# Performance work log

Hardware: AMD Instinct MI355X
Metric: run time of the kernel (lower is better)

## Reference

```python
import jax, jax.numpy as jnp
import numpy as np

RESO = 64            # plane_resolution
PADDING = 0.1
HID = 128            # hidden_dim
CDIM = 128           # c_dim
NBLOCKS = 5
PLANES = ((0, 2), (0, 1), (1, 2))  # xz, xy, yz column picks


def _plane_index(p, cols):
    # normalize_coordinate + coordinate2index (2d)
    xy = p[..., list(cols)] / (1.0 + PADDING + 1e-3) + 0.5
    xy = jnp.clip(xy, 0.0, 1.0 - 1e-3)
    ij = (xy * RESO).astype(jnp.int32)
    return ij[..., 0] + RESO * ij[..., 1]  # [B, T]


def _flat_idx(idx, S):
    B = idx.shape[0]
    return (idx + jnp.arange(B, dtype=idx.dtype)[:, None] * S).reshape(-1)


def _scatter_max(src, idx, S):
    # src [B,T,F], idx [B,T] -> [B,S,F]; empty bins -> 0 (torch_scatter convention)
    B, T, F = src.shape
    m = jax.ops.segment_max(src.reshape(B * T, F), _flat_idx(idx, S), num_segments=B * S)
    m = jnp.where(jnp.isfinite(m), m, jnp.zeros((), src.dtype))
    return m.reshape(B, S, F)


def _scatter_mean(src, idx, S):
    B, T, F = src.shape
    flat = _flat_idx(idx, S)
    s = jax.ops.segment_sum(src.reshape(B * T, F), flat, num_segments=B * S)
    cnt = jax.ops.segment_sum(jnp.ones((B * T,), src.dtype), flat, num_segments=B * S)
    return (s / jnp.maximum(cnt, 1.0)[:, None]).reshape(B, S, F)


def _resblock(x, w0, b0, w1, b1, ws):
    # ONet ResnetBlockFC: fc_1(relu(fc_0(relu(x)))) + shortcut(x)
    net = jax.nn.relu(x) @ w0 + b0
    dx = jax.nn.relu(net) @ w1 + b1
    return x @ ws + dx


def setup_inputs() -> dict:
    key = jax.random.key(0)
    ks = jax.random.split(key, 10)
    sc = 0.05
    return {
        "p": jax.random.normal(ks[0], (8, 20000, 3), dtype=jnp.float32),
        "fc_pos_w": jax.random.normal(ks[1], (3, 2 * HID), dtype=jnp.float32) * sc,
        "fc_pos_b": jnp.zeros((2 * HID,), jnp.float32),
        "blk0_w": jax.random.normal(ks[2], (NBLOCKS, 2 * HID, HID), dtype=jnp.float32) * sc,
        "blk0_b": jnp.zeros((NBLOCKS, HID), jnp.float32),
        "blk1_w": jax.random.normal(ks[3], (NBLOCKS, HID, HID), dtype=jnp.float32) * sc,
        "blk1_b": jnp.zeros((NBLOCKS, HID), jnp.float32),
        "blk_sc_w": jax.random.normal(ks[4], (NBLOCKS, 2 * HID, HID), dtype=jnp.float32) * sc,
        "fc_c_w": jax.random.normal(ks[5], (HID, CDIM), dtype=jnp.float32) * sc,
        "fc_c_b": jnp.zeros((CDIM,), jnp.float32),
    }


def reference(p, fc_pos_w, fc_pos_b, blk0_w, blk0_b, blk1_w, blk1_b, blk_sc_w, fc_c_w, fc_c_b):
    S = RESO * RESO
    B = p.shape[0]
    idxs = [_plane_index(p, cols) for cols in PLANES]

    net = p @ fc_pos_w + fc_pos_b                         # [B,T,2H]
    net = _resblock(net, blk0_w[0], blk0_b[0], blk1_w[0], blk1_b[0], blk_sc_w[0])
    for i in range(1, NBLOCKS):
        pooled = jnp.zeros_like(net[..., :HID])
        for idx in idxs:
            fea = _scatter_max(net, idx, S)               # [B,S,H]
            pooled = pooled + jnp.take_along_axis(fea, idx[:, :, None], axis=1)
        net = jnp.concatenate([net, pooled], axis=-1)     # [B,T,2H]
        net = _resblock(net, blk0_w[i], blk0_b[i], blk1_w[i], blk1_b[i], blk_sc_w[i])

    c = net @ fc_c_w + fc_c_b                             # [B,T,C]
    feas = []
    for idx in idxs:
        fp = _scatter_mean(c, idx, S)                     # [B,S,C]
        feas.append(fp.transpose(0, 2, 1).reshape(B, CDIM, RESO, RESO))
    return jnp.stack(feas)                                # [3,B,C,R,R] (xz, xy, yz)
```

## Files before the change

### kernel.cpp

```cpp
#include <hip/hip_runtime.h>
#include <cstdint>
#include <cstddef>

#define NP     160000
#define NB     8
#define TPB    20000
#define H      128
#define SS     4096
#define NCHUNK 625
#define NBLK   10
#define PPB    2000
#define NTILE  2500
#define GRIDP  1024

typedef _Float16 half8  __attribute__((ext_vector_type(8)));
typedef _Float16 half4v __attribute__((ext_vector_type(4)));
typedef float    f32x16 __attribute__((ext_vector_type(16)));

__device__ __forceinline__ half8 reluh8(half8 x) {
  half8 z = (half8)(_Float16)0;
  return __builtin_elementwise_max(x, z);
}

__global__ __launch_bounds__(256) void k_hist(const float* __restrict__ p,
                                              int* __restrict__ idx,
                                              unsigned* __restrict__ hist) {
  __shared__ unsigned lh[SS];
  const int tid = threadIdx.x;
  const int plb = blockIdx.x % 24;
  const int blk = blockIdx.x / 24;
  const int pl = plb >> 3, b = plb & 7;
  for (int j = tid; j < SS; j += 256) lh[j] = 0;
  __syncthreads();
  const float DEN = (float)(1.0 + 0.1 + 1e-3);
  const float HI  = (float)(1.0 - 1e-3);
  const int nbase = b*TPB + blk*PPB;
  for (int j = tid; j < PPB; j += 256) {
    const int n = nbase + j;
    const float px = p[3*n], py = p[3*n+1], pz = p[3*n+2];
    float ca, cb;
    if (pl == 0)      { ca = px; cb = pz; }
    else if (pl == 1) { ca = px; cb = py; }
    else              { ca = py; cb = pz; }
    const float na = fminf(fmaxf(ca / DEN + 0.5f, 0.0f), HI);
    const float nb = fminf(fmaxf(cb / DEN + 0.5f, 0.0f), HI);
    const int bin = (int)(na * 64.0f) + 64 * (int)(nb * 64.0f);
    idx[pl*NP + n] = bin;
    atomicAdd(&lh[bin], 1u);
  }
  __syncthreads();
  unsigned* dst = hist + ((size_t)plb*NBLK + blk)*SS;
  for (int j = tid; j < SS; j += 256) dst[j] = lh[j];
}

__global__ __launch_bounds__(256) void k_scan2(unsigned* __restrict__ hist,
                                               unsigned* __restrict__ cnt,
                                               int* __restrict__ cursor) {
  __shared__ unsigned stot[SS];
  __shared__ unsigned ssum[256];
  __shared__ unsigned sbase[256];
  const int plb = blockIdx.x;
  const int tid = threadIdx.x;
  unsigned* hp = hist + (size_t)plb*NBLK*SS;
  for (int j = tid; j < SS; j += 256) {
    unsigned t = 0;
    #pragma unroll
    for (int blk = 0; blk < NBLK; ++blk) t += hp[blk*SS + j];
    stot[j] = t;
  }
  __syncthreads();
  unsigned local = 0;
  #pragma unroll
  for (int i = 0; i < 16; ++i) local += stot[tid*16 + i];
  ssum[tid] = local;
  __syncthreads();
  if (tid == 0) {
    unsigned run = 0;
    for (int i = 0; i < 256; ++i) { sbase[i] = run; run += ssum[i]; }
  }
  __syncthreads();
  unsigned run = sbase[tid];
  for (int i = 0; i < 16; ++i) {
    const int bin = tid*16 + i;
    const unsigned tot = stot[bin];
    cnt[plb*SS + bin] = tot;
    cursor[plb*SS + bin] = (int)(run + tot);
    unsigned acc = run;
    #pragma unroll
    for (int blk = 0; blk < NBLK; ++blk) {
      const unsigned c = hp[blk*SS + bin];
      hp[blk*SS + bin] = acc;
      acc += c;
    }
    run += tot;
  }
}

__global__ __launch_bounds__(256) void k_reorder2(const int* __restrict__ idx,
                                                  const unsigned* __restrict__ hist,
                                                  int* __restrict__ order) {
  __shared__ unsigned lrank[SS];
  const int tid = threadIdx.x;
  const int plb = blockIdx.x % 24;
  const int blk = blockIdx.x / 24;
  const int pl = plb >> 3, b = plb & 7;
  for (int j = tid; j < SS; j += 256) lrank[j] = 0;
  __syncthreads();
  const unsigned* bp = hist + ((size_t)plb*NBLK + blk)*SS;
  int* op = order + pl*NP + b*TPB;
  const int nbase = b*TPB + blk*PPB;
  for (int j = tid; j < PPB; j += 256) {
    const int n = nbase + j;
    const int bin = idx[pl*NP + n];
    const unsigned r = atomicAdd(&lrank[bin], 1u);
    op[bp[bin] + r] = (bin << 18) | n;
  }
}

__global__ __launch_bounds__(256) void k_wconv(const float* __restrict__ w0,
                                               const float* __restrict__ w1,
                                               const float* __restrict__ wsc,
                                               _Float16* __restrict__ wb) {
  int t = blockIdx.x*256 + threadIdx.x;
  if (t >= 51200) return;
  int L = t / 10240, r = t % 10240;
  const float* src; _Float16* dst; int q;
  if (r < 4096)      { q = r;        src = w0  + L*32768; dst = wb + L*81920;         }
  else if (r < 8192) { q = r - 4096; src = wsc + L*32768; dst = wb + L*81920 + 32768; }
  else               { q = r - 8192; src = w1  + L*16384; dst = wb + L*81920 + 65536; }
  int kt = q >> 8, nt = (q >> 6) & 3, l = q & 63;
  int k0 = kt*16 + ((l >> 5) << 3);
  int n  = nt*32 + (l & 31);
  union { _Float16 h[8]; uint4 u; } o;
  #pragma unroll
  for (int j = 0; j < 8; ++j) o.h[j] = (_Float16)src[(size_t)(k0 + j)*H + n];
  *(uint4*)(dst + (size_t)q*8) = o.u;
}

template<int OP>
__global__ __launch_bounds__(256) void k_poolA(const _Float16* __restrict__ net,
                                               const int* __restrict__ order,
                                               _Float16* __restrict__ fea,
                                               float* __restrict__ sums,
                                               float* __restrict__ pbufF,
                                               float* __restrict__ pbufL) {
  const int tid   = threadIdx.x;
  const int plb   = blockIdx.x % 24;
  const int chunk = (blockIdx.x / 24) * 8 + (tid >> 5);
  if (chunk >= NCHUNK) return;
  const int gi = tid & 31, f4 = gi << 2;
  const int pl = plb >> 3, b = plb & 7;
  const int base = pl*NP + b*TPB + chunk*32;
  const int pkv = order[base + gi];
  const int prevbin = (chunk > 0)          ? (order[base - 1] >> 18) : -1;
  const int nextbin = (chunk < NCHUNK - 1) ? (order[base + 32] >> 18) : -1;

  uint2 v[32];
  #pragma unroll
  for (int i = 0; i < 32; ++i) {
    const int pk = __shfl(pkv, i, 32);
    v[i] = *(const uint2*)&net[(size_t)(pk & 0x3FFFF)*H + f4];
  }
  __builtin_amdgcn_sched_barrier(0);

  const size_t pslot = ((size_t)plb*NCHUNK + chunk)*H + f4;
  int cur = __shfl(pkv, 0, 32) >> 18;
  int segstart = 0;
  float a0, a1, a2, a3;
  if (OP == 0) { a0 = a1 = a2 = a3 = -3.0e38f; } else { a0 = a1 = a2 = a3 = 0.f; }

  #pragma unroll
  for (int i = 0; i < 32; ++i) {
    const int bin = __shfl(pkv, i, 32) >> 18;
    if (bin != cur) {
      const bool contin = (segstart == 0) && (prevbin == cur);
      if (!contin) {
        if (OP == 0) {
          union { _Float16 h[4]; uint2 u; } o;
          o.h[0]=(_Float16)a0; o.h[1]=(_Float16)a1; o.h[2]=(_Float16)a2; o.h[3]=(_Float16)a3;
          *(uint2*)&fea[((size_t)plb*SS + cur)*H + f4] = o.u;
        } else {
          *(float4*)&sums[((size_t)plb*SS + cur)*H + f4] = make_float4(a0,a1,a2,a3);
        }
      } else {
        *(float4*)&pbufF[pslot] = make_float4(a0,a1,a2,a3);
      }
      cur = bin; segstart = i;
      if (OP == 0) { a0 = a1 = a2 = a3 = -3.0e38f; } else { a0 = a1 = a2 = a3 = 0.f; }
    }
    union { uint2 u; _Float16 h[4]; } w;
    w.u = v[i];
    if (OP == 0) {
      a0 = fmaxf(a0, (float)w.h[0]); a1 = fmaxf(a1, (float)w.h[1]);
      a2 = fmaxf(a2, (float)w.h[2]); a3 = fmaxf(a3, (float)w.h[3]);
    } else {
      a0 += (float)w.h[0]; a1 += (float)w.h[1];
      a2 += (float)w.h[2]; a3 += (float)w.h[3];
    }
  }
  const bool contin = (segstart == 0) && (prevbin == cur);
  const bool extend = (nextbin == cur);
  if (!contin && !extend) {
    if (OP == 0) {
      union { _Float16 h[4]; uint2 u; } o;
      o.h[0]=(_Float16)a0; o.h[1]=(_Float16)a1; o.h[2]=(_Float16)a2; o.h[3]=(_Float16)a3;
      *(uint2*)&fea[((size_t)plb*SS + cur)*H + f4] = o.u;
    } else {
      *(float4*)&sums[((size_t)plb*SS + cur)*H + f4] = make_float4(a0,a1,a2,a3);
    }
  } else if (contin) {
    *(float4*)&pbufF[pslot] = make_float4(a0,a1,a2,a3);
  } else {
    *(float4*)&pbufL[pslot] = make_float4(a0,a1,a2,a3);
  }
}

template<int OP>
__global__ __launch_bounds__(256) void k_poolB(const int* __restrict__ order,
                                               const int* __restrict__ cursor,
                                               _Float16* __restrict__ fea,
                                               float* __restrict__ sums,
                                               const float* __restrict__ pbufF,
                                               const float* __restrict__ pbufL) {
  const int tid = threadIdx.x;
  const int plb = blockIdx.x % 24;
  const int bnd = (blockIdx.x / 24) * 8 + (tid >> 5);
  if (bnd >= NCHUNK - 1) return;
  const int gi = tid & 31, f4 = gi << 2;
  const int pl = plb >> 3, b = plb & 7;
  const int base = pl*NP + b*TPB;
  const int pos  = (bnd + 1) * 32;
  const int binR = order[base + pos] >> 18;
  const int binL = order[base + pos - 1] >> 18;
  if (binL != binR) return;
  const int beta = binR;
  const int e = cursor[plb*SS + beta];
  const int s = (beta > 0) ? cursor[plb*SS + beta - 1] : 0;
  const int cs = s >> 5, ce = (e - 1) >> 5;
  if (cs != bnd) return;
  float4 acc = *(const float4*)&pbufL[((size_t)plb*NCHUNK + cs)*H + f4];
  #pragma unroll 4
  for (int c = cs + 1; c <= ce; ++c) {
    const float4 q = *(const float4*)&pbufF[((size_t)plb*NCHUNK + c)*H + f4];
    if (OP == 0) {
      acc.x = fmaxf(acc.x, q.x); acc.y = fmaxf(acc.y, q.y);
      acc.z = fmaxf(acc.z, q.z); acc.w = fmaxf(acc.w, q.w);
    } else {
      acc.x += q.x; acc.y += q.y; acc.z += q.z; acc.w += q.w;
    }
  }
  if (OP == 0) {
    union { _Float16 h[4]; uint2 u; } o;
    o.h[0]=(_Float16)acc.x; o.h[1]=(_Float16)acc.y;
    o.h[2]=(_Float16)acc.z; o.h[3]=(_Float16)acc.w;
    *(uint2*)&fea[((size_t)plb*SS + beta)*H + f4] = o.u;
  } else {
    *(float4*)&sums[((size_t)plb*SS + beta)*H + f4] = acc;
  }
}

template<int MODE>
__global__ __launch_bounds__(256, 4) void k_block(
    const float* __restrict__ p,
    const float* __restrict__ wpos, const float* __restrict__ bpos,
    _Float16* __restrict__ net,
    const _Float16* __restrict__ fea, const int* __restrict__ idx,
    const _Float16* __restrict__ wb,
    const float* __restrict__ b0, const float* __restrict__ b1)
{
  __shared__ char smem[32768];
  char* Xs = smem;
  char* Hs = smem;
  const int tid = threadIdx.x;

  const int w  = tid >> 6;
  const int ln = tid & 63;
  const int l5 = ln >> 5;
  const int lr = ln & 31;
  const int sw = lr << 4;
  const int a0b = lr*512 + l5*16;
  const int a1b = a0b + 32*512;
  const int col = w*32 + lr;
  const int sw1 = (lr & 15) << 4;
  const float bb0 = b0[col];
  const float bb1 = b1[col];
  const _Float16* wb0 = wb;
  const _Float16* wbs = wb + 32768;
  const _Float16* wb1 = wb + 65536;

  for (int t = blockIdx.x; t < NTILE; t += gridDim.x) {
    const int n0 = t * 64;
    if (t != (int)blockIdx.x) __syncthreads();

    if (MODE == 0) {
      for (int j = tid; j < 64*64; j += 256) {
        int pt = j >> 6, k4 = (j & 63) << 2;
        int n = n0 + pt;
        float px = p[3*n], py = p[3*n+1], pz = p[3*n+2];
        float4 a  = *(const float4*)&bpos[k4];
        float4 wx = *(const float4*)&wpos[k4];
        float4 wy = *(const float4*)&wpos[256 + k4];
        float4 wz = *(const float4*)&wpos[512 + k4];
        a.x += px*wx.x + py*wy.x + pz*wz.x;
        a.y += px*wx.y + py*wy.y + pz*wz.y;
        a.z += px*wx.z + py*wy.z + pz*wz.z;
        a.w += px*wx.w + py*wy.w + pz*wz.w;
        union { _Float16 h[4]; uint2 u; } o;
        o.h[0] = (_Float16)a.x; o.h[1] = (_Float16)a.y;
        o.h[2] = (_Float16)a.z; o.h[3] = (_Float16)a.w;
        *(uint2*)(Xs + ((pt*512 + k4*2) ^ ((pt & 31) << 4))) = o.u;
      }
    } else {
      for (int j = tid; j < 64*32; j += 256) {
        int pt = j >> 5, k4 = (j & 31) << 2;
        int n = n0 + pt;
        int b = n / TPB;
        uint2 vleft = *(const uint2*)&net[(size_t)n*H + k4];
        union { uint2 u; half4v h; } w0g, w1g, w2g, o;
        w0g.u = *(const uint2*)&fea[(((size_t)(0*NB + b))*SS + idx[0*NP + n])*H + k4];
        w1g.u = *(const uint2*)&fea[(((size_t)(1*NB + b))*SS + idx[1*NP + n])*H + k4];
        w2g.u = *(const uint2*)&fea[(((size_t)(2*NB + b))*SS + idx[2*NP + n])*H + k4];
        o.h = (w0g.h + w1g.h) + w2g.h;
        const int swp = (pt & 31) << 4;
        *(uint2*)(Xs + ((pt*512 + k4*2) ^ swp)) = vleft;
        *(uint2*)(Xs + ((pt*512 + 256 + k4*2) ^ swp)) = o.u;
      }
    }
    __syncthreads();

    f32x16 aR0 = {}, aR1 = {}, aS0 = {}, aS1 = {};

    #pragma unroll 4
    for (int kt = 0; kt < 16; ++kt) {
      half8 x0 = *(const half8*)(Xs + ((a0b + kt*32) ^ sw));
      half8 x1 = *(const half8*)(Xs + ((a1b + kt*32) ^ sw));
      half8 r0 = reluh8(x0);
      half8 r1 = reluh8(x1);
      half8 bw = *(const half8*)(wb0 + ((kt*4 + w)*64 + ln)*8);
      half8 bs = *(const half8*)(wbs + ((kt*4 + w)*64 + ln)*8);
      aR0 = __builtin_amdgcn_mfma_f32_32x32x16_f16(r0, bw, aR0, 0, 0, 0);
      aR1 = __builtin_amdgcn_mfma_f32_32x32x16_f16(r1, bw, aR1, 0, 0, 0);
      aS0 = __builtin_amdgcn_mfma_f32_32x32x16_f16(x0, bs, aS0, 0, 0, 0);
      aS1 = __builtin_amdgcn_mfma_f32_32x32x16_f16(x1, bs, aS1, 0, 0, 0);
    }
    __syncthreads();

    #pragma unroll
    for (int reg = 0; reg < 16; ++reg) {
      int ro = (reg & 3) + 8*(reg >> 2) + 4*l5;
      float v0 = fmaxf(aR0[reg] + bb0, 0.f);
      float v1 = fmaxf(aR1[reg] + bb0, 0.f);
      *(_Float16*)(Hs + ((ro*256 + col*2) ^ ((ro & 15) << 4)))      = (_Float16)v0;
      *(_Float16*)(Hs + (((32+ro)*256 + col*2) ^ ((ro & 15) << 4))) = (_Float16)v1;
    }
    __syncthreads();

    #pragma unroll 2
    for (int kt = 0; kt < 8; ++kt) {
      half8 h0 = *(const half8*)(Hs + ((lr*256 + l5*16 + kt*32) ^ sw1));
      half8 h1 = *(const half8*)(Hs + (((32+lr)*256 + l5*16 + kt*32) ^ sw1));
      half8 bf = *(const half8*)(wb1 + ((kt*4 + w)*64 + ln)*8);
      aS0 = __builtin_amdgcn_mfma_f32_32x32x16_f16(h0, bf, aS0, 0, 0, 0);
      aS1 = __builtin_amdgcn_mfma_f32_32x32x16_f16(h1, bf, aS1, 0, 0, 0);
    }

    #pragma unroll
    for (int reg = 0; reg < 16; ++reg) {
      int ro = (reg & 3) + 8*(reg >> 2) + 4*l5;
      net[(size_t)(n0 + ro)*H + col]      = (_Float16)(aS0[reg] + bb1);
      net[(size_t)(n0 + 32 + ro)*H + col] = (_Float16)(aS1[reg] + bb1);
    }
  }
}

__global__ __launch_bounds__(256) void k_out2(const float* __restrict__ sums,
                                              const unsigned* __restrict__ cnt,
                                              const float* __restrict__ wc,
                                              const float* __restrict__ bc,
                                              float* __restrict__ out) {
  __shared__ float xa[64][132];
  const int plb = blockIdx.y;
  const int s0  = blockIdx.x << 6;
  const int tid = threadIdx.x;

  for (int j = tid; j < 64*32; j += 256) {
    int si = j >> 5, k4 = (j & 31) << 2;
    int s = s0 + si;
    float4 v = *(const float4*)&sums[((size_t)plb*SS + s)*H + k4];
    unsigned c = cnt[(size_t)plb*SS + s];
    float m = (c > 0u) ? (1.0f / (float)c) : 0.0f;
    xa[si][k4+0] = v.x*m; xa[si][k4+1] = v.y*m;
    xa[si][k4+2] = v.z*m; xa[si][k4+3] = v.w*m;
  }
  __syncthreads();

  const int fg = tid & 31;
  const int pg = tid >> 5;
  const int f4c = fg << 2;
  const int prow = pg << 3;
  float ac[8][4];
  #pragma unroll
  for (int i = 0; i < 8; ++i) { ac[i][0]=ac[i][1]=ac[i][2]=ac[i][3]=0.f; }
  #pragma unroll 4
  for (int k = 0; k < H; ++k) {
    const float4 wv = *(const float4*)&wc[(size_t)k*H + f4c];
    #pragma unroll
    for (int i = 0; i < 8; ++i) {
      const float xv = xa[prow + i][k];
      ac[i][0] += xv*wv.x; ac[i][1] += xv*wv.y; ac[i][2] += xv*wv.z; ac[i][3] += xv*wv.w;
    }
  }
  __syncthreads();
  const float4 bv = *(const float4*)&bc[f4c];
  #pragma unroll
  for (int i = 0; i < 8; ++i) {
    float4 o;
    o.x = ac[i][0] + bv.x;
    o.y = ac[i][1] + bv.y;
    o.z = ac[i][2] + bv.z;
    o.w = ac[i][3] + bv.w;
    *(float4*)&xa[prow + i][f4c] = o;
  }
  __syncthreads();

  for (int j = tid; j < H * 16; j += 256) {
    const int ch = j >> 4;
    const int s4 = (j & 15) << 2;
    float4 o;
    o.x = xa[s4 + 0][ch];
    o.y = xa[s4 + 1][ch];
    o.z = xa[s4 + 2][ch];
    o.w = xa[s4 + 3][ch];
    *(float4*)&out[((size_t)plb*H + ch)*SS + s0 + s4] = o;
  }
}

extern "C" void kernel_launch(void* const* d_in, const int* in_sizes, int n_in,
                              void* d_out, int out_size, void* d_ws, size_t ws_size,
                              hipStream_t stream) {
  (void)in_sizes; (void)n_in; (void)out_size; (void)ws_size;
  const float* p      = (const float*)d_in[0];
  const float* wpos   = (const float*)d_in[1];
  const float* bpos   = (const float*)d_in[2];
  const float* blk0w  = (const float*)d_in[3];
  const float* blk0b  = (const float*)d_in[4];
  const float* blk1w  = (const float*)d_in[5];
  const float* blk1b  = (const float*)d_in[6];
  const float* blkscw = (const float*)d_in[7];
  const float* wc     = (const float*)d_in[8];
  const float* bc     = (const float*)d_in[9];
  float* out = (float*)d_out;

  char* ws = (char*)d_ws;
  _Float16* net  = (_Float16*)ws;
  int* idx       = (int*)(ws + 40960000);
  int* order     = (int*)(ws + 42880000);
  int* cursor    = (int*)(ws + 44800000);
  unsigned* cnt  = (unsigned*)(ws + 45193216);
  _Float16* wb   = (_Float16*)(ws + 45586432);
  float* sums    = (float*)(ws + 46405632);
  float* pbufF   = (float*)(ws + 96737280);
  float* pbufL   = (float*)(ws + 104417280);
  unsigned* hist = (unsigned*)(ws + 112097280);
  _Float16* fea  = (_Float16*)d_out;

  k_hist<<<24*NBLK, 256, 0, stream>>>(p, idx, hist);
  k_scan2<<<24, 256, 0, stream>>>(hist, cnt, cursor);
  k_reorder2<<<24*NBLK, 256, 0, stream>>>(idx, hist, order);
  k_wconv<<<200, 256, 0, stream>>>(blk0w, blk1w, blkscw, wb);

  k_block<0><<<GRIDP, 256, 0, stream>>>(p, wpos, bpos, net, nullptr, idx,
                                        wb, blk0b, blk1b);

  for (int i = 1; i < 5; ++i) {
    k_poolA<0><<<79*24, 256, 0, stream>>>(net, order, fea, nullptr, pbufF, pbufL);
    k_poolB<0><<<78*24, 256, 0, stream>>>(order, cursor, fea, nullptr, pbufF, pbufL);
    k_block<1><<<GRIDP, 256, 0, stream>>>(nullptr, nullptr, nullptr, net, fea, idx,
                                          wb + (size_t)i*81920,
                                          blk0b + (size_t)i*H,
                                          blk1b + (size_t)i*H);
  }

  k_poolA<1><<<79*24, 256, 0, stream>>>(net, order, nullptr, sums, pbufF, pbufL);
  k_poolB<1><<<78*24, 256, 0, stream>>>(order, cursor, nullptr, sums, pbufF, pbufL);
  k_out2<<<dim3(64, 24), 256, 0, stream>>>(sums, cnt, wc, bc, out);
}
```

Measured before the change: 519.5 us.

## Restructure resblock kernel to one tile per 512-thread block with 8 waves

Replaces the persistent grid-stride k_block (256 threads, 4 waves each computing 64 rows with two accumulator pairs) with one 64-point tile per 512-thread block, where 8 waves each own a 32x32 output sub-tile. Separate LDS regions for X and H remove one barrier, and the fc_0 result is written to H before the shortcut GEMM runs. The aim is to cut per-wave register pressure and raise occupancy and latency hiding. In exchange every wave reloads the X tile for both GEMMs, LDS use grows to 48KB per block, and there are more block launches with no weight reuse across tiles.

```diff
diff --git a/kernel.cpp b/kernel.cpp
--- a/kernel.cpp
+++ b/kernel.cpp
@@ -10,8 +10,6 @@
 #define NCHUNK 625
 #define NBLK   10
 #define PPB    2000
-#define NTILE  2500
-#define GRIDP  1024
 
 typedef _Float16 half8  __attribute__((ext_vector_type(8)));
 typedef _Float16 half4v __attribute__((ext_vector_type(4)));
@@ -260,7 +258,7 @@
 }
 
 template<int MODE>
-__global__ __launch_bounds__(256, 4) void k_block(
+__global__ __launch_bounds__(512, 6) void k_block(
     const float* __restrict__ p,
     const float* __restrict__ wpos, const float* __restrict__ bpos,
     _Float16* __restrict__ net,
@@ -268,108 +266,101 @@
     const _Float16* __restrict__ wb,
     const float* __restrict__ b0, const float* __restrict__ b1)
 {
-  __shared__ char smem[32768];
+  __shared__ char smem[49152];
   char* Xs = smem;
-  char* Hs = smem;
-  const int tid = threadIdx.x;
+  char* Hs = smem + 32768;
+  const int tid = threadIdx.x;
+  const int n0  = blockIdx.x * 64;
+
+  if (MODE == 0) {
+    for (int j = tid; j < 64*64; j += 512) {
+      int pt = j >> 6, k4 = (j & 63) << 2;
+      int n = n0 + pt;
+      float px = p[3*n], py = p[3*n+1], pz = p[3*n+2];
+      float4 a  = *(const float4*)&bpos[k4];
+      float4 wx = *(const float4*)&wpos[k4];
+      float4 wy = *(const float4*)&wpos[256 + k4];
+      float4 wz = *(const float4*)&wpos[512 + k4];
+      a.x += px*wx.x + py*wy.x + pz*wz.x;
+      a.y += px*wx.y + py*wy.y + pz*wz.y;
+      a.z += px*wx.z + py*wy.z + pz*wz.z;
+      a.w += px*wx.w + py*wy.w + pz*wz.w;
+      union { _Float16 h[4]; uint2 u; } o;
+      o.h[0] = (_Float16)a.x; o.h[1] = (_Float16)a.y;
+      o.h[2] = (_Float16)a.z; o.h[3] = (_Float16)a.w;
+      *(uint2*)(Xs + ((pt*512 + k4*2) ^ ((pt & 31) << 4))) = o.u;
+    }
+  } else {
+    for (int j = tid; j < 64*32; j += 512) {
+      int pt = j >> 5, k4 = (j & 31) << 2;
+      int n = n0 + pt;
+      int b = n / TPB;
+      uint2 vleft = *(const uint2*)&net[(size_t)n*H + k4];
+      union { uint2 u; half4v h; } w0g, w1g, w2g, o;
+      w0g.u = *(const uint2*)&fea[(((size_t)(0*NB + b))*SS + idx[0*NP + n])*H + k4];
+      w1g.u = *(const uint2*)&fea[(((size_t)(1*NB + b))*SS + idx[1*NP + n])*H + k4];
+      w2g.u = *(const uint2*)&fea[(((size_t)(2*NB + b))*SS + idx[2*NP + n])*H + k4];
+      o.h = (w0g.h + w1g.h) + w2g.h;
+      const int sw = (pt & 31) << 4;
+      *(uint2*)(Xs + ((pt*512 + k4*2) ^ sw)) = vleft;
+      *(uint2*)(Xs + ((pt*512 + 256 + k4*2) ^ sw)) = o.u;
+    }
+  }
+  __syncthreads();
 
   const int w  = tid >> 6;
+  const int c  = w & 3;
+  const int r  = w >> 2;
   const int ln = tid & 63;
   const int l5 = ln >> 5;
   const int lr = ln & 31;
-  const int sw = lr << 4;
-  const int a0b = lr*512 + l5*16;
-  const int a1b = a0b + 32*512;
-  const int col = w*32 + lr;
-  const int sw1 = (lr & 15) << 4;
-  const float bb0 = b0[col];
-  const float bb1 = b1[col];
+  const int swx   = lr << 4;
+  const int xbase = lr*512 + l5*16 + r*16384;
+  const int col   = c*32 + lr;
   const _Float16* wb0 = wb;
   const _Float16* wbs = wb + 32768;
   const _Float16* wb1 = wb + 65536;
 
-  for (int t = blockIdx.x; t < NTILE; t += gridDim.x) {
-    const int n0 = t * 64;
-    if (t != (int)blockIdx.x) __syncthreads();
-
-    if (MODE == 0) {
-      for (int j = tid; j < 64*64; j += 256) {
-        int pt = j >> 6, k4 = (j & 63) << 2;
-        int n = n0 + pt;
-        float px = p[3*n], py = p[3*n+1], pz = p[3*n+2];
-        float4 a  = *(const float4*)&bpos[k4];
-        float4 wx = *(const float4*)&wpos[k4];
-        float4 wy = *(const float4*)&wpos[256 + k4];
-        float4 wz = *(const float4*)&wpos[512 + k4];
-        a.x += px*wx.x + py*wy.x + pz*wz.x;
-        a.y += px*wx.y + py*wy.y + pz*wz.y;
-        a.z += px*wx.z + py*wy.z + pz*wz.z;
-        a.w += px*wx.w + py*wy.w + pz*wz.w;
-        union { _Float16 h[4]; uint2 u; } o;
-        o.h[0] = (_Float16)a.x; o.h[1] = (_Float16)a.y;
-        o.h[2] = (_Float16)a.z; o.h[3] = (_Float16)a.w;
-        *(uint2*)(Xs + ((pt*512 + k4*2) ^ ((pt & 31) << 4))) = o.u;
-      }
-    } else {
-      for (int j = tid; j < 64*32; j += 256) {
-        int pt = j >> 5, k4 = (j & 31) << 2;
-        int n = n0 + pt;
-        int b = n / TPB;
-        uint2 vleft = *(const uint2*)&net[(size_t)n*H + k4];
-        union { uint2 u; half4v h; } w0g, w1g, w2g, o;
-        w0g.u = *(const uint2*)&fea[(((size_t)(0*NB + b))*SS + idx[0*NP + n])*H + k4];
-        w1g.u = *(const uint2*)&fea[(((size_t)(1*NB + b))*SS + idx[1*NP + n])*H + k4];
-        w2g.u = *(const uint2*)&fea[(((size_t)(2*NB + b))*SS + idx[2*NP + n])*H + k4];
-        o.h = (w0g.h + w1g.h) + w2g.h;
-        const int swp = (pt & 31) << 4;
-        *(uint2*)(Xs + ((pt*512 + k4*2) ^ swp)) = vleft;
-        *(uint2*)(Xs + ((pt*512 + 256 + k4*2) ^ swp)) = o.u;
-      }
-    }
-    __syncthreads();
-
-    f32x16 aR0 = {}, aR1 = {}, aS0 = {}, aS1 = {};
-
-    #pragma unroll 4
-    for (int kt = 0; kt < 16; ++kt) {
-      half8 x0 = *(const half8*)(Xs + ((a0b + kt*32) ^ sw));
-      half8 x1 = *(const half8*)(Xs + ((a1b + kt*32) ^ sw));
-      half8 r0 = reluh8(x0);
-      half8 r1 = reluh8(x1);
-      half8 bw = *(const half8*)(wb0 + ((kt*4 + w)*64 + ln)*8);
-      half8 bs = *(const half8*)(wbs + ((kt*4 + w)*64 + ln)*8);
-      aR0 = __builtin_amdgcn_mfma_f32_32x32x16_f16(r0, bw, aR0, 0, 0, 0);
-      aR1 = __builtin_amdgcn_mfma_f32_32x32x16_f16(r1, bw, aR1, 0, 0, 0);
-      aS0 = __builtin_amdgcn_mfma_f32_32x32x16_f16(x0, bs, aS0, 0, 0, 0);
-      aS1 = __builtin_amdgcn_mfma_f32_32x32x16_f16(x1, bs, aS1, 0, 0, 0);
-    }
-    __syncthreads();
-
-    #pragma unroll
-    for (int reg = 0; reg < 16; ++reg) {
-      int ro = (reg & 3) + 8*(reg >> 2) + 4*l5;
-      float v0 = fmaxf(aR0[reg] + bb0, 0.f);
-      float v1 = fmaxf(aR1[reg] + bb0, 0.f);
-      *(_Float16*)(Hs + ((ro*256 + col*2) ^ ((ro & 15) << 4)))      = (_Float16)v0;
-      *(_Float16*)(Hs + (((32+ro)*256 + col*2) ^ ((ro & 15) << 4))) = (_Float16)v1;
-    }
-    __syncthreads();
-
-    #pragma unroll 2
-    for (int kt = 0; kt < 8; ++kt) {
-      half8 h0 = *(const half8*)(Hs + ((lr*256 + l5*16 + kt*32) ^ sw1));
-      half8 h1 = *(const half8*)(Hs + (((32+lr)*256 + l5*16 + kt*32) ^ sw1));
-      half8 bf = *(const half8*)(wb1 + ((kt*4 + w)*64 + ln)*8);
-      aS0 = __builtin_amdgcn_mfma_f32_32x32x16_f16(h0, bf, aS0, 0, 0, 0);
-      aS1 = __builtin_amdgcn_mfma_f32_32x32x16_f16(h1, bf, aS1, 0, 0, 0);
-    }
-
-    #pragma unroll
-    for (int reg = 0; reg < 16; ++reg) {
-      int ro = (reg & 3) + 8*(reg >> 2) + 4*l5;
-      net[(size_t)(n0 + ro)*H + col]      = (_Float16)(aS0[reg] + bb1);
-      net[(size_t)(n0 + 32 + ro)*H + col] = (_Float16)(aS1[reg] + bb1);
-    }
+  f32x16 aR = {};
+  #pragma unroll 4
+  for (int kt = 0; kt < 16; ++kt) {
+    half8 x  = *(const half8*)(Xs + ((xbase + kt*32) ^ swx));
+    half8 rx = reluh8(x);
+    half8 bw = *(const half8*)(wb0 + ((kt*4 + c)*64 + ln)*8);
+    aR = __builtin_amdgcn_mfma_f32_32x32x16_f16(rx, bw, aR, 0, 0, 0);
+  }
+  const float bb0 = b0[col];
+  #pragma unroll
+  for (int reg = 0; reg < 16; ++reg) {
+    const int ro  = (reg & 3) + 8*(reg >> 2) + 4*l5;
+    const int row = r*32 + ro;
+    const float v = fmaxf(aR[reg] + bb0, 0.f);
+    *(_Float16*)(Hs + ((row*256 + col*2) ^ ((row & 15) << 4))) = (_Float16)v;
+  }
+
+  f32x16 aS = {};
+  #pragma unroll 4
+  for (int kt = 0; kt < 16; ++kt) {
+    half8 x  = *(const half8*)(Xs + ((xbase + kt*32) ^ swx));
+    half8 bs = *(const half8*)(wbs + ((kt*4 + c)*64 + ln)*8);
+    aS = __builtin_amdgcn_mfma_f32_32x32x16_f16(x, bs, aS, 0, 0, 0);
+  }
+  __syncthreads();
+
+  const int hbase = (r*32 + lr)*256 + l5*16;
+  const int swh   = (lr & 15) << 4;
+  #pragma unroll 2
+  for (int kt = 0; kt < 8; ++kt) {
+    half8 h  = *(const half8*)(Hs + ((hbase + kt*32) ^ swh));
+    half8 bf = *(const half8*)(wb1 + ((kt*4 + c)*64 + ln)*8);
+    aS = __builtin_amdgcn_mfma_f32_32x32x16_f16(h, bf, aS, 0, 0, 0);
+  }
+
+  const float bb1 = b1[col];
+  #pragma unroll
+  for (int reg = 0; reg < 16; ++reg) {
+    const int ro = (reg & 3) + 8*(reg >> 2) + 4*l5;
+    net[(size_t)(n0 + r*32 + ro)*H + col] = (_Float16)(aS[reg] + bb1);
   }
 }
 
@@ -469,16 +460,16 @@
   k_reorder2<<<24*NBLK, 256, 0, stream>>>(idx, hist, order);
   k_wconv<<<200, 256, 0, stream>>>(blk0w, blk1w, blkscw, wb);
 
-  k_block<0><<<GRIDP, 256, 0, stream>>>(p, wpos, bpos, net, nullptr, idx,
-                                        wb, blk0b, blk1b);
+  k_block<0><<<2500, 512, 0, stream>>>(p, wpos, bpos, net, nullptr, idx,
+                                       wb, blk0b, blk1b);
 
   for (int i = 1; i < 5; ++i) {
     k_poolA<0><<<79*24, 256, 0, stream>>>(net, order, fea, nullptr, pbufF, pbufL);
     k_poolB<0><<<78*24, 256, 0, stream>>>(order, cursor, fea, nullptr, pbufF, pbufL);
-    k_block<1><<<GRIDP, 256, 0, stream>>>(nullptr, nullptr, nullptr, net, fea, idx,
-                                          wb + (size_t)i*81920,
-                                          blk0b + (size_t)i*H,
-                                          blk1b + (size_t)i*H);
+    k_block<1><<<2500, 512, 0, stream>>>(nullptr, nullptr, nullptr, net, fea, idx,
+                                         wb + (size_t)i*81920,
+                                         blk0b + (size_t)i*H,
+                                         blk1b + (size_t)i*H);
   }
 
   k_poolA<1><<<79*24, 256, 0, stream>>>(net, order, nullptr, sums, pbufF, pbufL);
```

Result: faster. 470.7 us, median of 2 (-9.4%).
